# Kernel optimization log

Hardware: AMD Instinct MI355X
Metric: run time of the kernel (lower is better)

The kernel has to match this reference:

```python
import jax, jax.numpy as jnp
import numpy as np

B, N, H, S, NSEC = 1, 8192, 256, 128, 8
TAU = 0.5
DEPTH_LO, DEPTH_HI = 0.0, 2.4
PADDING = 0.1
EPS = 1e-6
_p = float(np.clip(TAU, 1e-4, 1.0 - 1e-4))
LOGIT_TAU = float(np.log(_p / (1.0 - _p)))


def mlp(p, W1, b1, W2, b2, W3, b3, W4, b4):
    # p: [..., 3] -> logit [...]
    h = jax.nn.softplus(p @ W1 + b1)
    h = jax.nn.softplus(h @ W2 + b2)
    h = jax.nn.softplus(h @ W3 + b3)
    return (h @ W4 + b4)[..., 0]


def cube_intersection(ray0, rd):
    # Faithful port of check_ray_intersection_with_unit_cube.
    p_dist = 0.5 + PADDING / 2.0
    plane = jnp.concatenate([jnp.full((3,), p_dist), jnp.full((3,), -p_dist)])  # (6,)
    nom = plane - jnp.tile(ray0, (1, 1, 2))          # (B,N,6)
    den = jnp.tile(rd, (1, 1, 2))
    den = jnp.where(jnp.abs(den) < 1e-9, 1e-9, den)  # numerical guard
    d_int = nom / den                                 # (B,N,6)
    p_int = ray0[:, :, None, :] + d_int[..., None] * rd[:, :, None, :]  # (B,N,6,3)
    inside = jnp.all(jnp.abs(p_int) <= p_dist + EPS, axis=-1)           # (B,N,6)
    mask = inside.sum(-1) == 2                                           # rays hitting cube
    # pick the (exactly two) intersecting planes in ascending plane order,
    # matching torch boolean indexing semantics
    plane_id = jnp.arange(6)
    key = jnp.where(inside, plane_id, plane_id + 6)
    idx2 = jnp.argsort(key, axis=-1)[..., :2]                            # (B,N,2)
    p2 = jnp.take_along_axis(p_int, idx2[..., None], axis=2)            # (B,N,2,3)
    norm_rd = jnp.linalg.norm(rd, axis=-1)                               # (B,N)
    d2 = jnp.linalg.norm(p2 - ray0[:, :, None, :], axis=-1) / norm_rd[..., None]
    d2 = jnp.where(mask[..., None], d2, 0.0)
    d2 = jnp.sort(d2, axis=-1)
    return d2, mask


def _secant(d_low, f_low, d_high, f_high):
    den = f_high - f_low
    den = jnp.where(jnp.abs(den) < 1e-12, 1e-12, den)
    return -f_low * (d_high - d_low) / den + d_low


def reference(ray0, ray_direction, W1, b1, W2, b2, W3, b3, W4, b4):
    rd = ray_direction
    dec = lambda p: mlp(p, W1, b1, W2, b2, W3, b3, W4, b4)
    sg = jax.lax.stop_gradient

    # ---- proposal depths (no grad, as torch no_grad ray-marching) ----
    t = jnp.linspace(0.0, 1.0, S)                       # (S,)
    d_default = DEPTH_LO + t * (DEPTH_HI - DEPTH_LO)
    d2, mask_cube = cube_intersection(ray0, rd)
    d_cube = d2[..., 0:1] + t * (d2[..., 1:2] - d2[..., 0:1])   # (B,N,S)
    d_prop = jnp.where(mask_cube[..., None], d_cube, d_default)
    d_prop = sg(d_prop)

    p_prop = sg(ray0)[:, :, None, :] + d_prop[..., None] * sg(rd)[:, :, None, :]
    val = sg(dec(p_prop)) - LOGIT_TAU                   # (B,N,S)

    mask_0_not_occupied = val[..., 0] < 0
    sign_matrix = jnp.concatenate(
        [jnp.sign(val[..., :-1] * val[..., 1:]), jnp.ones(val.shape[:-1] + (1,), val.dtype)], -1)
    cost = sign_matrix * jnp.arange(S, 0, -1, dtype=val.dtype)
    idx = jnp.argmin(cost, -1)                          # first sign-change step
    vmin = jnp.min(cost, -1)
    f_low = jnp.take_along_axis(val, idx[..., None], -1)[..., 0]
    mask = (vmin < 0) & (f_low < 0) & mask_0_not_occupied

    idx_hi = jnp.minimum(idx + 1, S - 1)
    d_low = jnp.take_along_axis(d_prop, idx[..., None], -1)[..., 0]
    d_high = jnp.take_along_axis(d_prop, idx_hi[..., None], -1)[..., 0]
    f_high = jnp.take_along_axis(val, idx_hi[..., None], -1)[..., 0]

    # ---- secant refinement (no grad in torch) ----
    r0s, rds = sg(ray0), sg(rd)
    d_pred = _secant(d_low, f_low, d_high, f_high)
    for _ in range(NSEC):
        f_mid = sg(dec(r0s + d_pred[..., None] * rds)) - LOGIT_TAU
        low = f_mid < 0
        d_low = jnp.where(low, d_pred, d_low)
        f_low = jnp.where(low, f_mid, f_low)
        d_high = jnp.where(low, d_high, d_pred)
        f_high = jnp.where(low, f_high, f_mid)
        d_pred = _secant(d_low, f_low, d_high, f_high)

    # ---- differentiable implicit-gradient correction (analytic backward of
    # DepthFunction: dd/dtheta = -(df/dtheta)/(df/dd) at the surface point) ----
    d_star = sg(d_pred)
    f_of_d = lambda d: dec(ray0 + d[..., None] * rd) - LOGIT_TAU
    f_val = f_of_d(d_star)                              # differentiable wrt params/rays
    _, df_dd = jax.jvp(f_of_d, (d_star,), (jnp.ones_like(d_star),))
    df_dd = sg(df_dd)
    df_dd = jnp.where(jnp.abs(df_dd) < 1e-6,
                      jnp.where(df_dd < 0, -1e-6, 1e-6), df_dd)
    d_out = d_star - f_val / df_dd
    d_final = jnp.where(mask, d_out, 0.0)
    return d_final


def setup_inputs() -> dict:
    key = jax.random.key(0)
    ks = jax.random.split(key, 10)
    origin = jnp.array([0.0, 0.0, -1.5])
    ray0 = origin + 0.01 * jax.random.normal(ks[0], (B, N, 3), dtype=jnp.float32)
    target = jax.random.uniform(ks[1], (B, N, 3), minval=-0.4, maxval=0.4, dtype=jnp.float32)
    rd = target - ray0
    rd = rd / jnp.linalg.norm(rd, axis=-1, keepdims=True)
    W1 = jax.random.normal(ks[2], (3, H), dtype=jnp.float32) / jnp.sqrt(3.0)
    b1 = 0.1 * jax.random.normal(ks[3], (H,), dtype=jnp.float32)
    W2 = jax.random.normal(ks[4], (H, H), dtype=jnp.float32) / jnp.sqrt(float(H))
    b2 = 0.1 * jax.random.normal(ks[5], (H,), dtype=jnp.float32)
    W3 = jax.random.normal(ks[6], (H, H), dtype=jnp.float32) / jnp.sqrt(float(H))
    b3 = 0.1 * jax.random.normal(ks[7], (H,), dtype=jnp.float32)
    W4 = jax.random.normal(ks[8], (H, 1), dtype=jnp.float32) / jnp.sqrt(float(H))
    b4 = 0.1 * jax.random.normal(ks[9], (1,), dtype=jnp.float32)
    return {"ray0": ray0, "ray_direction": rd, "W1": W1, "b1": b1,
            "W2": W2, "b2": b2, "W3": W3, "b3": b3, "W4": W4, "b4": b4}
```

## Files before the change

### kernel.cpp

```cpp
#include <hip/hip_runtime.h>
#include <math.h>

#define NRAY 8192
#define SSAMP 128
#define HD 256
#define AROW 264
#define A1ROW 40
#define FIXCAP 262144
#define FIXTHR 0.018f

typedef short s16x8 __attribute__((ext_vector_type(8)));
typedef float f32x4 __attribute__((ext_vector_type(4)));

__device__ __forceinline__ unsigned short f2bf(float f) {
    unsigned u = __float_as_uint(f);
    u += 0x7fffu + ((u >> 16) & 1u);
    return (unsigned short)(u >> 16);
}
__device__ __forceinline__ float bf2f(unsigned short s) {
    return __uint_as_float(((unsigned)s) << 16);
}
__device__ __forceinline__ void split2(float f, unsigned short& hi, unsigned short& lo) {
    unsigned u = __float_as_uint(f);
    hi = (unsigned short)(u >> 16);
    float r = f - __uint_as_float(u & 0xFFFF0000u);
    lo = f2bf(r);
}
__device__ __forceinline__ float softplus_fast(float x) {
    return fmaxf(x, 0.0f) + __logf(1.0f + __expf(-fabsf(x)));
}
__device__ __forceinline__ float softplus_cheap(float x) {
    float m = __expf(-fabsf(x));
    float p = fmaf(m, fmaf(0.14258f, m, -0.44943f), 1.0f);
    return fmaxf(x, 0.0f) + m * p;
}
__device__ __forceinline__ float sigmoid_fast(float x) {
    return 1.0f / (1.0f + __expf(-x));
}

__global__ __launch_bounds__(256)
void prep_kernel(const float* __restrict__ W1, const float* __restrict__ b1,
                 const float* __restrict__ W2, const float* __restrict__ W3,
                 const float* __restrict__ ray0, const float* __restrict__ rdg,
                 unsigned short* __restrict__ P2, unsigned short* __restrict__ P3,
                 unsigned short* __restrict__ B1, float* __restrict__ rayinfo,
                 int* __restrict__ fix_cnt) {
    const int b = blockIdx.x, tid = threadIdx.x;
    if (b < 256) {
        int idx = b * 256 + tid;
        int k = idx >> 8, n = idx & 255;
        int nt = n >> 4, kt = k >> 5, lq = (k >> 3) & 3, j = k & 7;
        int lane = (lq << 4) | (n & 15);
        size_t off = (size_t)((nt * 8 + kt) * 2) * 512 + (size_t)lane * 8 + j;
        float w = W2[idx];
        unsigned short hi = f2bf(w);
        P2[off] = hi; P2[off + 512] = f2bf(w - bf2f(hi));
        w = W3[idx];
        hi = f2bf(w);
        P3[off] = hi; P3[off + 512] = f2bf(w - bf2f(hi));
    } else if (b < 288) {
        int idx = (b - 256) * 256 + tid;
        int w = idx & 511;
        int lane = w >> 3, j = w & 7;
        int k = ((lane >> 4) << 3) + j;
        int n = ((idx >> 9) << 4) + (lane & 15);
        unsigned short s = 0;
        if (k < 3) s = f2bf(W1[k * HD + n]);
        else if (k == 3) s = f2bf(b1[n]);
        else if (k < 7) s = f2bf(W1[(k - 4) * HD + n]);
        else if (k == 7) { unsigned short bh = f2bf(b1[n]); s = f2bf(b1[n] - bf2f(bh)); }
        else if (k < 11) { float wv = W1[(k - 8) * HD + n]; unsigned short wh = f2bf(wv); s = f2bf(wv - bf2f(wh)); }
        B1[idx] = s;
    } else {
        int r = (b - 288) * 256 + tid;
        if (r == 0) *fix_cnt = 0;
        float o0 = ray0[3 * r], o1 = ray0[3 * r + 1], o2 = ray0[3 * r + 2];
        float v0 = rdg[3 * r], v1 = rdg[3 * r + 1], v2 = rdg[3 * r + 2];
        const float pd = 0.55f, lim = pd + 1e-6f;
        float di[6]; int insk[6]; int cnt = 0;
        for (int k = 0; k < 6; k++) {
            int a = k % 3;
            float pl = (k < 3) ? pd : -pd;
            float den = (a == 0) ? v0 : ((a == 1) ? v1 : v2);
            if (fabsf(den) < 1e-9f) den = 1e-9f;
            float oa = (a == 0) ? o0 : ((a == 1) ? o1 : o2);
            float dd = (pl - oa) / den;
            float px = o0 + dd * v0, py = o1 + dd * v1, pz = o2 + dd * v2;
            int ins = (fabsf(px) <= lim) && (fabsf(py) <= lim) && (fabsf(pz) <= lim);
            di[k] = dd; insk[k] = ins; cnt += ins;
        }
        float d0 = 0.f, sl = 2.4f;
        if (cnt == 2) {
            int k1 = -1, k2 = -1;
            for (int k = 0; k < 6; k++) if (insk[k]) { if (k1 < 0) k1 = k; else k2 = k; }
            float nrd = sqrtf(v0 * v0 + v1 * v1 + v2 * v2);
            float ax = di[k1] * v0, ay = di[k1] * v1, az = di[k1] * v2;
            float d1n = sqrtf(ax * ax + ay * ay + az * az) / nrd;
            float bx = di[k2] * v0, by = di[k2] * v1, bz = di[k2] * v2;
            float d2n = sqrtf(bx * bx + by * by + bz * bz) / nrd;
            d0 = fminf(d1n, d2n);
            sl = fmaxf(d1n, d2n) - d0;
        }
        float* ri = rayinfo + (size_t)r * 8;
        ri[0] = d0; ri[1] = sl;
        ri[2] = o0; ri[3] = o1; ri[4] = o2;
        ri[5] = v0; ri[6] = v1; ri[7] = v2;
    }
}

template<int MT>
__device__ __forceinline__ void gemm_l1(const unsigned short* A1,
                                        const unsigned short* __restrict__ B1,
                                        f32x4 acc[MT][4], int lane, int ntbase) {
    const int r15 = lane & 15, q = lane >> 4;
    s16x8 bh[4];
#pragma unroll
    for (int nt = 0; nt < 4; nt++)
        bh[nt] = *(((const s16x8*)B1) + (size_t)(ntbase + nt) * 64 + lane);
#pragma unroll
    for (int mt = 0; mt < MT; mt++) {
        s16x8 ah = *(const s16x8*)(A1 + (mt * 16 + r15) * A1ROW + q * 8);
#pragma unroll
        for (int nt = 0; nt < 4; nt++)
            acc[mt][nt] = __builtin_amdgcn_mfma_f32_16x16x32_bf16(ah, bh[nt], (f32x4){0.f,0.f,0.f,0.f}, 0, 0, 0);
    }
}

template<int MT>
__device__ __forceinline__ void gemm_1t(const unsigned short* Ahi,
                                        const unsigned short* __restrict__ Bp,
                                        f32x4 acc[MT][4], int lane, int ntbase) {
#pragma unroll
    for (int mt = 0; mt < MT; mt++)
#pragma unroll
        for (int nt = 0; nt < 4; nt++) acc[mt][nt] = (f32x4){0.f, 0.f, 0.f, 0.f};
    const int r15 = lane & 15, q = lane >> 4;
#pragma unroll 2
    for (int kt = 0; kt < 8; kt++) {
        s16x8 bh[4];
#pragma unroll
        for (int nt = 0; nt < 4; nt++) {
            const s16x8* bp = ((const s16x8*)Bp) + (size_t)((ntbase + nt) * 8 + kt) * 128 + lane;
            bh[nt] = bp[0];
        }
        const int kc = kt * 32 + q * 8;
#pragma unroll
        for (int mt = 0; mt < MT; mt++) {
            s16x8 ah = *(const s16x8*)(Ahi + (mt * 16 + r15) * AROW + kc);
#pragma unroll
            for (int nt = 0; nt < 4; nt++)
                acc[mt][nt] = __builtin_amdgcn_mfma_f32_16x16x32_bf16(ah, bh[nt], acc[mt][nt], 0, 0, 0);
        }
    }
}

template<int MT>
__device__ __forceinline__ void gemm_3t(const unsigned short* Ahi, const unsigned short* Alo,
                                        const unsigned short* __restrict__ Bp,
                                        f32x4 acc[MT][4], int lane, int ntbase) {
#pragma unroll
    for (int mt = 0; mt < MT; mt++)
#pragma unroll
        for (int nt = 0; nt < 4; nt++) acc[mt][nt] = (f32x4){0.f, 0.f, 0.f, 0.f};
    const int r15 = lane & 15, q = lane >> 4;
#pragma unroll 2
    for (int kt = 0; kt < 8; kt++) {
        s16x8 bh[4], bl[4];
#pragma unroll
        for (int nt = 0; nt < 4; nt++) {
            const s16x8* bp = ((const s16x8*)Bp) + (size_t)((ntbase + nt) * 8 + kt) * 128 + lane;
            bh[nt] = bp[0];
            bl[nt] = bp[64];
        }
        const int kc = kt * 32 + q * 8;
#pragma unroll
        for (int mt = 0; mt < MT; mt++) {
            s16x8 ah = *(const s16x8*)(Ahi + (mt * 16 + r15) * AROW + kc);
            s16x8 al = *(const s16x8*)(Alo + (mt * 16 + r15) * AROW + kc);
#pragma unroll
            for (int nt = 0; nt < 4; nt++) {
                acc[mt][nt] = __builtin_amdgcn_mfma_f32_16x16x32_bf16(ah, bh[nt], acc[mt][nt], 0, 0, 0);
                acc[mt][nt] = __builtin_amdgcn_mfma_f32_16x16x32_bf16(ah, bl[nt], acc[mt][nt], 0, 0, 0);
                acc[mt][nt] = __builtin_amdgcn_mfma_f32_16x16x32_bf16(al, bh[nt], acc[mt][nt], 0, 0, 0);
            }
        }
    }
}

template<int MT>
__device__ __forceinline__ void gemm_dual(const unsigned short* Avh, const unsigned short* Avl,
                                          const unsigned short* Ath, const unsigned short* Atl,
                                          const unsigned short* __restrict__ Bp,
                                          f32x4 av[MT][4], f32x4 at[MT][4], int lane, int ntbase) {
#pragma unroll
    for (int mt = 0; mt < MT; mt++)
#pragma unroll
        for (int nt = 0; nt < 4; nt++) {
            av[mt][nt] = (f32x4){0.f, 0.f, 0.f, 0.f};
            at[mt][nt] = (f32x4){0.f, 0.f, 0.f, 0.f};
        }
    const int r15 = lane & 15, q = lane >> 4;
#pragma unroll 2
    for (int kt = 0; kt < 8; kt++) {
        s16x8 bh[4], bl[4];
#pragma unroll
        for (int nt = 0; nt < 4; nt++) {
            const s16x8* bp = ((const s16x8*)Bp) + (size_t)((ntbase + nt) * 8 + kt) * 128 + lane;
            bh[nt] = bp[0];
            bl[nt] = bp[64];
        }
        const int kc = kt * 32 + q * 8;
#pragma unroll
        for (int mt = 0; mt < MT; mt++) {
            s16x8 avh = *(const s16x8*)(Avh + (mt * 16 + r15) * AROW + kc);
            s16x8 avl = *(const s16x8*)(Avl + (mt * 16 + r15) * AROW + kc);
            s16x8 ath = *(const s16x8*)(Ath + (mt * 16 + r15) * AROW + kc);
            s16x8 atl = *(const s16x8*)(Atl + (mt * 16 + r15) * AROW + kc);
#pragma unroll
            for (int nt = 0; nt < 4; nt++) {
                av[mt][nt] = __builtin_amdgcn_mfma_f32_16x16x32_bf16(avh, bh[nt], av[mt][nt], 0, 0, 0);
                av[mt][nt] = __builtin_amdgcn_mfma_f32_16x16x32_bf16(avh, bl[nt], av[mt][nt], 0, 0, 0);
                av[mt][nt] = __builtin_amdgcn_mfma_f32_16x16x32_bf16(avl, bh[nt], av[mt][nt], 0, 0, 0);
                at[mt][nt] = __builtin_amdgcn_mfma_f32_16x16x32_bf16(ath, bh[nt], at[mt][nt], 0, 0, 0);
                at[mt][nt] = __builtin_amdgcn_mfma_f32_16x16x32_bf16(ath, bl[nt], at[mt][nt], 0, 0, 0);
                at[mt][nt] = __builtin_amdgcn_mfma_f32_16x16x32_bf16(atl, bh[nt], at[mt][nt], 0, 0, 0);
            }
        }
    }
}

template<int MT>
__device__ __forceinline__ void epi_l1(f32x4 acc[MT][4], unsigned short* Ahi, int lane, int wn0) {
    const int r15 = lane & 15, q = lane >> 4;
#pragma unroll
    for (int mt = 0; mt < MT; mt++)
#pragma unroll
        for (int nt = 0; nt < 4; nt++) {
            int col = wn0 + nt * 16 + r15;
#pragma unroll
            for (int reg = 0; reg < 4; reg++) {
                int row = mt * 16 + q * 4 + reg;
                Ahi[row * AROW + col] = f2bf(softplus_cheap(acc[mt][nt][reg]));
            }
        }
}

template<int MT>
__device__ __forceinline__ void epi_l1_sp(f32x4 acc[MT][4], unsigned short* Ahi, unsigned short* Alo,
                                          int lane, int wn0) {
    const int r15 = lane & 15, q = lane >> 4;
#pragma unroll
    for (int mt = 0; mt < MT; mt++)
#pragma unroll
        for (int nt = 0; nt < 4; nt++) {
            int col = wn0 + nt * 16 + r15;
#pragma unroll
            for (int reg = 0; reg < 4; reg++) {
                int row = mt * 16 + q * 4 + reg;
                float h = softplus_fast(acc[mt][nt][reg]);
                unsigned short hi, lo;
                split2(h, hi, lo);
                Ahi[row * AROW + col] = hi;
                Alo[row * AROW + col] = lo;
            }
        }
}

template<int MT>
__device__ __forceinline__ void epi_hidden_1t(f32x4 acc[MT][4], const float* __restrict__ b,
                                              unsigned short* Ahi, int lane, int wn0) {
    const int r15 = lane & 15, q = lane >> 4;
#pragma unroll
    for (int mt = 0; mt < MT; mt++)
#pragma unroll
        for (int nt = 0; nt < 4; nt++) {
            int col = wn0 + nt * 16 + r15;
            float bb = b[col];
#pragma unroll
            for (int reg = 0; reg < 4; reg++) {
                int row = mt * 16 + q * 4 + reg;
                Ahi[row * AROW + col] = f2bf(softplus_cheap(acc[mt][nt][reg] + bb));
            }
        }
}

template<int MT>
__device__ __forceinline__ void epi_hidden_sp(f32x4 acc[MT][4], const float* __restrict__ b,
                                              unsigned short* Ahi, unsigned short* Alo,
                                              int lane, int wn0) {
    const int r15 = lane & 15, q = lane >> 4;
#pragma unroll
    for (int mt = 0; mt < MT; mt++)
#pragma unroll
        for (int nt = 0; nt < 4; nt++) {
            int col = wn0 + nt * 16 + r15;
            float bb = b[col];
#pragma unroll
            for (int reg = 0; reg < 4; reg++) {
                int row = mt * 16 + q * 4 + reg;
                float h = softplus_fast(acc[mt][nt][reg] + bb);
                unsigned short hi, lo;
                split2(h, hi, lo);
                Ahi[row * AROW + col] = hi;
                Alo[row * AROW + col] = lo;
            }
        }
}

template<int MT>
__device__ __forceinline__ void epi_dual(f32x4 av[MT][4], f32x4 at[MT][4], const float* __restrict__ b,
                                         unsigned short* Avh, unsigned short* Avl,
                                         unsigned short* Ath, unsigned short* Atl,
                                         int lane, int wn0) {
    const int r15 = lane & 15, q = lane >> 4;
#pragma unroll
    for (int mt = 0; mt < MT; mt++)
#pragma unroll
        for (int nt = 0; nt < 4; nt++) {
            int col = wn0 + nt * 16 + r15;
            float bb = b[col];
#pragma unroll
            for (int reg = 0; reg < 4; reg++) {
                int row = mt * 16 + q * 4 + reg;
                float z = av[mt][nt][reg] + bb;
                float h = softplus_fast(z);
                float ht = sigmoid_fast(z) * at[mt][nt][reg];
                unsigned short hi, lo;
                split2(h, hi, lo);
                Avh[row * AROW + col] = hi;
                Avl[row * AROW + col] = lo;
                split2(ht, hi, lo);
                Ath[row * AROW + col] = hi;
                Atl[row * AROW + col] = lo;
            }
        }
}

template<int MT, bool CH>
__device__ __forceinline__ void l4_reduce(f32x4 acc[MT][4], const float* __restrict__ b3,
                                          const float* __restrict__ W4,
                                          float* partial, int lane, int wn0) {
    const int r15 = lane & 15, q = lane >> 4;
    float w4v[4], b3v[4];
#pragma unroll
    for (int nt = 0; nt < 4; nt++) {
        int col = wn0 + nt * 16 + r15;
        w4v[nt] = W4[col]; b3v[nt] = b3[col];
    }
#pragma unroll
    for (int mt = 0; mt < MT; mt++)
#pragma unroll
        for (int reg = 0; reg < 4; reg++) {
            float p = 0.f;
#pragma unroll
            for (int nt = 0; nt < 4; nt++) {
                float z = acc[mt][nt][reg] + b3v[nt];
                float h = CH ? softplus_cheap(z) : softplus_fast(z);
                p += h * w4v[nt];
            }
#pragma unroll
            for (int m = 1; m < 16; m <<= 1) p += __shfl_xor(p, m, 64);
            if (r15 == 0) partial[mt * 16 + q * 4 + reg] = p;
        }
}

template<int MT>
__device__ __forceinline__ void l4_reduce_dual(f32x4 av[MT][4], f32x4 at[MT][4],
                                               const float* __restrict__ b3, const float* __restrict__ W4,
                                               float* pv, float* pt, int lane, int wn0) {
    const int r15 = lane & 15, q = lane >> 4;
    float w4v[4], b3v[4];
#pragma unroll
    for (int nt = 0; nt < 4; nt++) {
        int col = wn0 + nt * 16 + r15;
        w4v[nt] = W4[col]; b3v[nt] = b3[col];
    }
#pragma unroll
    for (int mt = 0; mt < MT; mt++)
#pragma unroll
        for (int reg = 0; reg < 4; reg++) {
            float sv = 0.f, st = 0.f;
#pragma unroll
            for (int nt = 0; nt < 4; nt++) {
                float z = av[mt][nt][reg] + b3v[nt];
                sv += softplus_fast(z) * w4v[nt];
                st += sigmoid_fast(z) * at[mt][nt][reg] * w4v[nt];
            }
#pragma unroll
            for (int m = 1; m < 16; m <<= 1) {
                sv += __shfl_xor(sv, m, 64);
                st += __shfl_xor(st, m, 64);
            }
            if (r15 == 0) {
                pv[mt * 16 + q * 4 + reg] = sv;
                pt[mt * 16 + q * 4 + reg] = st;
            }
        }
}

__global__ __launch_bounds__(256, 4)
void coarse_mfma(const float* __restrict__ rayinfo,
                 const unsigned short* __restrict__ B1,
                 const unsigned short* __restrict__ P2, const float* __restrict__ b2,
                 const unsigned short* __restrict__ P3, const float* __restrict__ b3,
                 const float* __restrict__ W4, const float* __restrict__ b4,
                 float* __restrict__ val_out, float* __restrict__ dprop_out,
                 int* __restrict__ fix_cnt, int* __restrict__ fix_list) {
    __shared__ __align__(16) unsigned short Ahi[64 * AROW];
    __shared__ __align__(16) unsigned short A1[64 * A1ROW];
    float* partial = (float*)A1;
    const int tid = threadIdx.x;
    const int lane = tid & 63, wave = tid >> 6;
    const int r = blockIdx.x >> 1, half = blockIdx.x & 1;

    if (tid < 64) {
        const float* ri = rayinfo + (size_t)r * 8;
        const int s = half * 64 + tid;
        float t = (float)s * (1.0f / 127.0f);
        float d = fmaf(t, ri[1], ri[0]);
        dprop_out[r * SSAMP + s] = d;
        float px = fmaf(d, ri[5], ri[2]);
        float py = fmaf(d, ri[6], ri[3]);
        float pz = fmaf(d, ri[7], ri[4]);
        unsigned short hx, lx, hy, ly, hz, lz;
        split2(px, hx, lx); split2(py, hy, ly); split2(pz, hz, lz);
        unsigned short* row = A1 + tid * A1ROW;
        row[0] = hx; row[1] = hy; row[2] = hz; row[3] = 0x3F80u;
        row[4] = lx; row[5] = ly; row[6] = lz; row[7] = 0x3F80u;
        row[8] = hx; row[9] = hy; row[10] = hz;
#pragma unroll
        for (int c = 11; c < 32; c++) row[c] = 0;
    }
    __syncthreads();
    f32x4 acc[4][4];
    gemm_l1<4>(A1, B1, acc, lane, wave * 4);
    epi_l1<4>(acc, Ahi, lane, wave * 64);
    __syncthreads();
    gemm_1t<4>(Ahi, P2, acc, lane, wave * 4);
    __syncthreads();
    epi_hidden_1t<4>(acc, b2, Ahi, lane, wave * 64);
    __syncthreads();
    gemm_1t<4>(Ahi, P3, acc, lane, wave * 4);
    l4_reduce<4, true>(acc, b3, W4, &partial[wave * 64], lane, wave * 64);
    __syncthreads();
    if (tid < 64) {
        float v = partial[tid] + partial[64 + tid] + partial[128 + tid] + partial[192 + tid] + b4[0];
        int idx = r * SSAMP + half * 64 + tid;
        val_out[idx] = v;
        if (fabsf(v) < FIXTHR) {
            int pos = atomicAdd(fix_cnt, 1);
            if (pos < FIXCAP) fix_list[pos] = idx;
        }
    }
}

__global__ __launch_bounds__(256, 4)
void fixup3_mfma(const int* __restrict__ counter, const int* __restrict__ list,
                 float* __restrict__ val, const float* __restrict__ dprop,
                 const float* __restrict__ ray0, const float* __restrict__ rdg,
                 const unsigned short* __restrict__ B1,
                 const unsigned short* __restrict__ P2, const float* __restrict__ b2,
                 const unsigned short* __restrict__ P3, const float* __restrict__ b3,
                 const float* __restrict__ W4, const float* __restrict__ b4) {
    __shared__ __align__(16) unsigned short Ahi[32 * AROW];
    __shared__ __align__(16) unsigned short Alo[32 * AROW];
    __shared__ __align__(16) unsigned short A1[32 * A1ROW];
    __shared__ float partial[4][32];
    __shared__ int bidxs[32];
    const int cnt = min(*counter, FIXCAP);
    const int base = blockIdx.x * 32;
    if (base >= cnt) return;
    const int tid = threadIdx.x;
    const int lane = tid & 63, wave = tid >> 6;
    if (tid < 32) {
        const int i = min(base + tid, cnt - 1);
        const int bidx = list[i];
        bidxs[tid] = bidx;
        const int rr = bidx >> 7;
        float d = dprop[bidx];
        float px = ray0[3 * rr] + d * rdg[3 * rr];
        float py = ray0[3 * rr + 1] + d * rdg[3 * rr + 1];
        float pz = ray0[3 * rr + 2] + d * rdg[3 * rr + 2];
        unsigned short hx, lx, hy, ly, hz, lz;
        split2(px, hx, lx); split2(py, hy, ly); split2(pz, hz, lz);
        unsigned short* row = A1 + tid * A1ROW;
        row[0] = hx; row[1] = hy; row[2] = hz; row[3] = 0x3F80u;
        row[4] = lx; row[5] = ly; row[6] = lz; row[7] = 0x3F80u;
        row[8] = hx; row[9] = hy; row[10] = hz;
#pragma unroll
        for (int c = 11; c < 32; c++) row[c] = 0;
    }
    __syncthreads();
    f32x4 acc[2][4];
    gemm_l1<2>(A1, B1, acc, lane, wave * 4);
    epi_l1_sp<2>(acc, Ahi, Alo, lane, wave * 64);
    __syncthreads();
    gemm_3t<2>(Ahi, Alo, P2, acc, lane, wave * 4);
    __syncthreads();
    epi_hidden_sp<2>(acc, b2, Ahi, Alo, lane, wave * 64);
    __syncthreads();
    gemm_3t<2>(Ahi, Alo, P3, acc, lane, wave * 4);
    l4_reduce<2, false>(acc, b3, W4, &partial[wave][0], lane, wave * 64);
    __syncthreads();
    if (tid < 32) {
        float v = partial[0][tid] + partial[1][tid] + partial[2][tid] + partial[3][tid] + b4[0];
        val[bidxs[tid]] = v;
    }
}

__global__ __launch_bounds__(256, 4)
void refine_mfma(const float* __restrict__ val, const float* __restrict__ dprop,
                 const float* __restrict__ ray0, const float* __restrict__ rdg,
                 const float* __restrict__ W1, const float* __restrict__ b1,
                 const unsigned short* __restrict__ P2, const float* __restrict__ b2,
                 const unsigned short* __restrict__ P3, const float* __restrict__ b3,
                 const float* __restrict__ W4, const float* __restrict__ b4,
                 float* __restrict__ out) {
    __shared__ __align__(16) unsigned short Avh[16 * AROW];
    __shared__ __align__(16) unsigned short Avl[16 * AROW];
    __shared__ __align__(16) unsigned short Ath[16 * AROW];
    __shared__ __align__(16) unsigned short Atl[16 * AROW];
    __shared__ float partial[4][16], ptan[4][16];
    __shared__ float dl[16], fl[16], dh[16], fh[16], dps[16];
    __shared__ int mks[16];
    unsigned short* Ahi = Avh;
    const int tid = threadIdx.x;
    const int lane = tid & 63, wave = tid >> 6;
    const int r0 = blockIdx.x * 16;

    for (int i = 0; i < 4; i++) {
        const int r = r0 + wave * 4 + i;
        const float2 v = *(const float2*)(val + (size_t)r * SSAMP + lane * 2);
        const float2 dd = *(const float2*)(dprop + (size_t)r * SSAMP + lane * 2);
        float vnext = __shfl_down(v.x, 1, 64);
        const int s0 = lane * 2, s1 = s0 + 1;
        float pr0 = v.x * v.y;
        int sg0 = (pr0 > 0.f) ? 1 : ((pr0 < 0.f) ? -1 : 0);
        int k0 = (sg0 * (SSAMP - s0) + 129) * 256 + s0;
        int k1;
        if (lane == 63) {
            k1 = (1 + 129) * 256 + 127;
        } else {
            float pr1 = v.y * vnext;
            int sg1 = (pr1 > 0.f) ? 1 : ((pr1 < 0.f) ? -1 : 0);
            k1 = (sg1 * (SSAMP - s1) + 129) * 256 + s1;
        }
        int k = min(k0, k1);
#pragma unroll
        for (int m = 1; m < 64; m <<= 1) k = min(k, __shfl_xor(k, m, 64));
        int bidx = k & 255;
        int cmin = (k >> 8) - 129;
        int idxh = min(bidx + 1, SSAMP - 1);
        int ow = bidx >> 1, oh = idxh >> 1;
        float fa = __shfl(v.x, ow, 64), fb = __shfl(v.y, ow, 64);
        float da = __shfl(dd.x, ow, 64), db = __shfl(dd.y, ow, 64);
        float fa2 = __shfl(v.x, oh, 64), fb2 = __shfl(v.y, oh, 64);
        float da2 = __shfl(dd.x, oh, 64), db2 = __shfl(dd.y, oh, 64);
        float v0 = __shfl(v.x, 0, 64);
        if (lane == 0) {
            float f_low = (bidx & 1) ? fb : fa;
            float d_low = (bidx & 1) ? db : da;
            float f_high = (idxh & 1) ? fb2 : fa2;
            float d_high = (idxh & 1) ? db2 : da2;
            int sl = wave * 4 + i;
            mks[sl] = (cmin < 0) && (f_low < 0.f) && (v0 < 0.f);
            float den = f_high - f_low;
            if (fabsf(den) < 1e-12f) den = 1e-12f;
            dl[sl] = d_low; fl[sl] = f_low; dh[sl] = d_high; fh[sl] = f_high;
            dps[sl] = -f_low * (d_high - d_low) / den + d_low;
        }
    }
    __syncthreads();
    for (int it = 0; it < 8; it++) {
        {
            const int pt = tid >> 4, jb = (tid & 15) << 4;
            const int rr = r0 + pt;
            float d = dps[pt];
            float px = ray0[3 * rr] + d * rdg[3 * rr];
            float py = ray0[3 * rr + 1] + d * rdg[3 * rr + 1];
            float pz = ray0[3 * rr + 2] + d * rdg[3 * rr + 2];
            for (int j = jb; j < jb + 16; j += 4) {
                float4 wa = *(const float4*)(W1 + j);
                float4 wb = *(const float4*)(W1 + 256 + j);
                float4 wc = *(const float4*)(W1 + 512 + j);
                float4 bb = *(const float4*)(b1 + j);
                float z[4];
                z[0] = fmaf(px, wa.x, fmaf(py, wb.x, fmaf(pz, wc.x, bb.x)));
                z[1] = fmaf(px, wa.y, fmaf(py, wb.y, fmaf(pz, wc.y, bb.y)));
                z[2] = fmaf(px, wa.z, fmaf(py, wb.z, fmaf(pz, wc.z, bb.z)));
                z[3] = fmaf(px, wa.w, fmaf(py, wb.w, fmaf(pz, wc.w, bb.w)));
#pragma unroll
                for (int i = 0; i < 4; i++)
                    Ahi[pt * AROW + j + i] = f2bf(softplus_cheap(z[i]));
            }
        }
        __syncthreads();
        f32x4 acc[1][4];
        gemm_1t<1>(Ahi, P2, acc, lane, wave * 4);
        __syncthreads();
        epi_hidden_1t<1>(acc, b2, Ahi, lane, wave * 64);
        __syncthreads();
        gemm_1t<1>(Ahi, P3, acc, lane, wave * 4);
        l4_reduce<1, true>(acc, b3, W4, &partial[wave][0], lane, wave * 64);
        __syncthreads();
        if (tid < 16) {
            float fm = partial[0][tid] + partial[1][tid] + partial[2][tid] + partial[3][tid] + b4[0];
            float dpv = dps[tid];
            float dlv = dl[tid], flv = fl[tid], dhv = dh[tid], fhv = fh[tid];
            if (fm < 0.f) { dlv = dpv; flv = fm; } else { dhv = dpv; fhv = fm; }
            float den = fhv - flv;
            if (fabsf(den) < 1e-12f) den = 1e-12f;
            dps[tid] = -flv * (dhv - dlv) / den + dlv;
            dl[tid] = dlv; fl[tid] = flv; dh[tid] = dhv; fh[tid] = fhv;
        }
        __syncthreads();
    }
    {
        const int pt = tid >> 4, jb = (tid & 15) << 4;
        const int rr = r0 + pt;
        float d = dps[pt];
        float v0 = rdg[3 * rr], v1 = rdg[3 * rr + 1], v2 = rdg[3 * rr + 2];
        float px = ray0[3 * rr] + d * v0;
        float py = ray0[3 * rr + 1] + d * v1;
        float pz = ray0[3 * rr + 2] + d * v2;
        for (int j = jb; j < jb + 16; j += 4) {
            float4 wa = *(const float4*)(W1 + j);
            float4 wb = *(const float4*)(W1 + 256 + j);
            float4 wc = *(const float4*)(W1 + 512 + j);
            float4 bb = *(const float4*)(b1 + j);
            float z[4], zt[4];
            z[0] = fmaf(px, wa.x, fmaf(py, wb.x, fmaf(pz, wc.x, bb.x)));
            z[1] = fmaf(px, wa.y, fmaf(py, wb.y, fmaf(pz, wc.y, bb.y)));
            z[2] = fmaf(px, wa.z, fmaf(py, wb.z, fmaf(pz, wc.z, bb.z)));
            z[3] = fmaf(px, wa.w, fmaf(py, wb.w, fmaf(pz, wc.w, bb.w)));
            zt[0] = fmaf(v0, wa.x, fmaf(v1, wb.x, v2 * wc.x));
            zt[1] = fmaf(v0, wa.y, fmaf(v1, wb.y, v2 * wc.y));
            zt[2] = fmaf(v0, wa.z, fmaf(v1, wb.z, v2 * wc.z));
            zt[3] = fmaf(v0, wa.w, fmaf(v1, wb.w, v2 * wc.w));
#pragma unroll
            for (int i = 0; i < 4; i++) {
                float h = softplus_fast(z[i]);
                float ht = sigmoid_fast(z[i]) * zt[i];
                unsigned short hi, lo;
                split2(h, hi, lo);
                Avh[pt * AROW + j + i] = hi;
                Avl[pt * AROW + j + i] = lo;
                split2(ht, hi, lo);
                Ath[pt * AROW + j + i] = hi;
                Atl[pt * AROW + j + i] = lo;
            }
        }
    }
    __syncthreads();
    f32x4 av[1][4], at[1][4];
    gemm_dual<1>(Avh, Avl, Ath, Atl, P2, av, at, lane, wave * 4);
    __syncthreads();
    epi_dual<1>(av, at, b2, Avh, Avl, Ath, Atl, lane, wave * 64);
    __syncthreads();
    gemm_dual<1>(Avh, Avl, Ath, Atl, P3, av, at, lane, wave * 4);
    l4_reduce_dual<1>(av, at, b3, W4, &partial[wave][0], &ptan[wave][0], lane, wave * 64);
    __syncthreads();
    if (tid < 16) {
        float f = partial[0][tid] + partial[1][tid] + partial[2][tid] + partial[3][tid] + b4[0];
        float ft = ptan[0][tid] + ptan[1][tid] + ptan[2][tid] + ptan[3][tid];
        if (fabsf(ft) < 1e-6f) ft = (ft < 0.f) ? -1e-6f : 1e-6f;
        float dres = dps[tid] - f / ft;
        out[r0 + tid] = mks[tid] ? dres : 0.0f;
    }
}

extern "C" void kernel_launch(void* const* d_in, const int* in_sizes, int n_in,
                              void* d_out, int out_size, void* d_ws, size_t ws_size,
                              hipStream_t stream) {
    const float* ray0 = (const float*)d_in[0];
    const float* rdg  = (const float*)d_in[1];
    const float* W1 = (const float*)d_in[2];
    const float* b1 = (const float*)d_in[3];
    const float* W2 = (const float*)d_in[4];
    const float* b2 = (const float*)d_in[5];
    const float* W3 = (const float*)d_in[6];
    const float* b3 = (const float*)d_in[7];
    const float* W4 = (const float*)d_in[8];
    const float* b4 = (const float*)d_in[9];
    float* out = (float*)d_out;

    float* ws = (float*)d_ws;
    float* val    = ws;
    float* dprop  = ws + (size_t)SSAMP * NRAY;
    unsigned short* P2 = (unsigned short*)(ws + (size_t)2 * SSAMP * NRAY);
    unsigned short* P3 = P2 + 131072;
    unsigned short* B1 = P3 + 131072;
    float* rayinfo = (float*)(B1 + 8192);
    int* fix_cnt  = (int*)(rayinfo + (size_t)NRAY * 8);
    int* fix_list = fix_cnt + 64;

    hipLaunchKernelGGL(prep_kernel, dim3(320), dim3(256), 0, stream,
                       W1, b1, W2, W3, ray0, rdg, P2, P3, B1, rayinfo, fix_cnt);
    hipLaunchKernelGGL(coarse_mfma, dim3(NRAY * 2), dim3(256), 0, stream,
                       rayinfo, B1, P2, b2, P3, b3, W4, b4, val, dprop, fix_cnt, fix_list);
    hipLaunchKernelGGL(fixup3_mfma, dim3(FIXCAP / 32), dim3(256), 0, stream,
                       fix_cnt, fix_list, val, dprop, ray0, rdg,
                       B1, P2, b2, P3, b3, W4, b4);
    hipLaunchKernelGGL(refine_mfma, dim3(NRAY / 16), dim3(256), 0, stream,
                       val, dprop, ray0, rdg, W1, b1, P2, b2, P3, b3, W4, b4, out);
}
```

Measured before the change: 726.3 us.

## Transpose MFMA operand order and vectorize epilogue stores with packed bf16 conversion

Swaps the A/B operands of every MFMA so each lane's accumulator holds four consecutive hidden columns of one row instead of four rows of one column. Epilogues can then write packed 64-bit stores to LDS using the hardware v_cvt_pk_bf16_f32 instruction in place of scalar 16-bit stores, and bias/W4 loads become vector loads. The final-layer reduction needs only two cross-lane shuffles instead of four. The change also alters bf16 rounding for the hi part (round-to-nearest instead of truncation), so the hi/lo split numerics differ slightly.

```diff
diff --git a/kernel.cpp b/kernel.cpp
--- a/kernel.cpp
+++ b/kernel.cpp
@@ -25,6 +25,11 @@
     hi = (unsigned short)(u >> 16);
     float r = f - __uint_as_float(u & 0xFFFF0000u);
     lo = f2bf(r);
+}
+__device__ __forceinline__ unsigned pack_bf16x2(float a, float b) {
+    unsigned r;
+    asm("v_cvt_pk_bf16_f32 %0, %1, %2" : "=v"(r) : "v"(a), "v"(b));
+    return r;
 }
 __device__ __forceinline__ float softplus_fast(float x) {
     return fmaxf(x, 0.0f) + __logf(1.0f + __expf(-fabsf(x)));
@@ -108,27 +113,28 @@
     }
 }
 
+
 template<int MT>
 __device__ __forceinline__ void gemm_l1(const unsigned short* A1,
                                         const unsigned short* __restrict__ B1,
                                         f32x4 acc[MT][4], int lane, int ntbase) {
     const int r15 = lane & 15, q = lane >> 4;
-    s16x8 bh[4];
+    s16x8 wh[4];
 #pragma unroll
     for (int nt = 0; nt < 4; nt++)
-        bh[nt] = *(((const s16x8*)B1) + (size_t)(ntbase + nt) * 64 + lane);
+        wh[nt] = *(((const s16x8*)B1) + (size_t)(ntbase + nt) * 64 + lane);
 #pragma unroll
     for (int mt = 0; mt < MT; mt++) {
         s16x8 ah = *(const s16x8*)(A1 + (mt * 16 + r15) * A1ROW + q * 8);
 #pragma unroll
         for (int nt = 0; nt < 4; nt++)
-            acc[mt][nt] = __builtin_amdgcn_mfma_f32_16x16x32_bf16(ah, bh[nt], (f32x4){0.f,0.f,0.f,0.f}, 0, 0, 0);
-    }
-}
-
-template<int MT>
-__device__ __forceinline__ void gemm_1t(const unsigned short* Ahi,
-                                        const unsigned short* __restrict__ Bp,
+            acc[mt][nt] = __builtin_amdgcn_mfma_f32_16x16x32_bf16(wh[nt], ah, (f32x4){0.f,0.f,0.f,0.f}, 0, 0, 0);
+    }
+}
+
+template<int MT>
+__device__ __forceinline__ void gemm_1t(const unsigned short* Act,
+                                        const unsigned short* __restrict__ Wp,
                                         f32x4 acc[MT][4], int lane, int ntbase) {
 #pragma unroll
     for (int mt = 0; mt < MT; mt++)
@@ -137,26 +143,26 @@
     const int r15 = lane & 15, q = lane >> 4;
 #pragma unroll 2
     for (int kt = 0; kt < 8; kt++) {
-        s16x8 bh[4];
-#pragma unroll
-        for (int nt = 0; nt < 4; nt++) {
-            const s16x8* bp = ((const s16x8*)Bp) + (size_t)((ntbase + nt) * 8 + kt) * 128 + lane;
-            bh[nt] = bp[0];
+        s16x8 wh[4];
+#pragma unroll
+        for (int nt = 0; nt < 4; nt++) {
+            const s16x8* wp = ((const s16x8*)Wp) + (size_t)((ntbase + nt) * 8 + kt) * 128 + lane;
+            wh[nt] = wp[0];
         }
         const int kc = kt * 32 + q * 8;
 #pragma unroll
         for (int mt = 0; mt < MT; mt++) {
-            s16x8 ah = *(const s16x8*)(Ahi + (mt * 16 + r15) * AROW + kc);
+            s16x8 ah = *(const s16x8*)(Act + (mt * 16 + r15) * AROW + kc);
 #pragma unroll
             for (int nt = 0; nt < 4; nt++)
-                acc[mt][nt] = __builtin_amdgcn_mfma_f32_16x16x32_bf16(ah, bh[nt], acc[mt][nt], 0, 0, 0);
+                acc[mt][nt] = __builtin_amdgcn_mfma_f32_16x16x32_bf16(wh[nt], ah, acc[mt][nt], 0, 0, 0);
         }
     }
 }
 
 template<int MT>
 __device__ __forceinline__ void gemm_3t(const unsigned short* Ahi, const unsigned short* Alo,
-                                        const unsigned short* __restrict__ Bp,
+                                        const unsigned short* __restrict__ Wp,
                                         f32x4 acc[MT][4], int lane, int ntbase) {
 #pragma unroll
     for (int mt = 0; mt < MT; mt++)
@@ -165,12 +171,12 @@
     const int r15 = lane & 15, q = lane >> 4;
 #pragma unroll 2
     for (int kt = 0; kt < 8; kt++) {
-        s16x8 bh[4], bl[4];
-#pragma unroll
-        for (int nt = 0; nt < 4; nt++) {
-            const s16x8* bp = ((const s16x8*)Bp) + (size_t)((ntbase + nt) * 8 + kt) * 128 + lane;
-            bh[nt] = bp[0];
-            bl[nt] = bp[64];
+        s16x8 wh[4], wl[4];
+#pragma unroll
+        for (int nt = 0; nt < 4; nt++) {
+            const s16x8* wp = ((const s16x8*)Wp) + (size_t)((ntbase + nt) * 8 + kt) * 128 + lane;
+            wh[nt] = wp[0];
+            wl[nt] = wp[64];
         }
         const int kc = kt * 32 + q * 8;
 #pragma unroll
@@ -179,9 +185,9 @@
             s16x8 al = *(const s16x8*)(Alo + (mt * 16 + r15) * AROW + kc);
 #pragma unroll
             for (int nt = 0; nt < 4; nt++) {
-                acc[mt][nt] = __builtin_amdgcn_mfma_f32_16x16x32_bf16(ah, bh[nt], acc[mt][nt], 0, 0, 0);
-                acc[mt][nt] = __builtin_amdgcn_mfma_f32_16x16x32_bf16(ah, bl[nt], acc[mt][nt], 0, 0, 0);
-                acc[mt][nt] = __builtin_amdgcn_mfma_f32_16x16x32_bf16(al, bh[nt], acc[mt][nt], 0, 0, 0);
+                acc[mt][nt] = __builtin_amdgcn_mfma_f32_16x16x32_bf16(wh[nt], ah, acc[mt][nt], 0, 0, 0);
+                acc[mt][nt] = __builtin_amdgcn_mfma_f32_16x16x32_bf16(wl[nt], ah, acc[mt][nt], 0, 0, 0);
+                acc[mt][nt] = __builtin_amdgcn_mfma_f32_16x16x32_bf16(wh[nt], al, acc[mt][nt], 0, 0, 0);
             }
         }
     }
@@ -190,7 +196,7 @@
 template<int MT>
 __device__ __forceinline__ void gemm_dual(const unsigned short* Avh, const unsigned short* Avl,
                                           const unsigned short* Ath, const unsigned short* Atl,
-                                          const unsigned short* __restrict__ Bp,
+                                          const unsigned short* __restrict__ Wp,
                                           f32x4 av[MT][4], f32x4 at[MT][4], int lane, int ntbase) {
 #pragma unroll
     for (int mt = 0; mt < MT; mt++)
@@ -202,28 +208,28 @@
     const int r15 = lane & 15, q = lane >> 4;
 #pragma unroll 2
     for (int kt = 0; kt < 8; kt++) {
-        s16x8 bh[4], bl[4];
-#pragma unroll
-        for (int nt = 0; nt < 4; nt++) {
-            const s16x8* bp = ((const s16x8*)Bp) + (size_t)((ntbase + nt) * 8 + kt) * 128 + lane;
-            bh[nt] = bp[0];
-            bl[nt] = bp[64];
+        s16x8 wh[4], wl[4];
+#pragma unroll
+        for (int nt = 0; nt < 4; nt++) {
+            const s16x8* wp = ((const s16x8*)Wp) + (size_t)((ntbase + nt) * 8 + kt) * 128 + lane;
+            wh[nt] = wp[0];
+            wl[nt] = wp[64];
         }
         const int kc = kt * 32 + q * 8;
 #pragma unroll
         for (int mt = 0; mt < MT; mt++) {
-            s16x8 avh = *(const s16x8*)(Avh + (mt * 16 + r15) * AROW + kc);
-            s16x8 avl = *(const s16x8*)(Avl + (mt * 16 + r15) * AROW + kc);
-            s16x8 ath = *(const s16x8*)(Ath + (mt * 16 + r15) * AROW + kc);
-            s16x8 atl = *(const s16x8*)(Atl + (mt * 16 + r15) * AROW + kc);
+            s16x8 avhf = *(const s16x8*)(Avh + (mt * 16 + r15) * AROW + kc);
+            s16x8 avlf = *(const s16x8*)(Avl + (mt * 16 + r15) * AROW + kc);
+            s16x8 athf = *(const s16x8*)(Ath + (mt * 16 + r15) * AROW + kc);
+            s16x8 atlf = *(const s16x8*)(Atl + (mt * 16 + r15) * AROW + kc);
 #pragma unroll
             for (int nt = 0; nt < 4; nt++) {
-                av[mt][nt] = __builtin_amdgcn_mfma_f32_16x16x32_bf16(avh, bh[nt], av[mt][nt], 0, 0, 0);
-                av[mt][nt] = __builtin_amdgcn_mfma_f32_16x16x32_bf16(avh, bl[nt], av[mt][nt], 0, 0, 0);
-                av[mt][nt] = __builtin_amdgcn_mfma_f32_16x16x32_bf16(avl, bh[nt], av[mt][nt], 0, 0, 0);
-                at[mt][nt] = __builtin_amdgcn_mfma_f32_16x16x32_bf16(ath, bh[nt], at[mt][nt], 0, 0, 0);
-                at[mt][nt] = __builtin_amdgcn_mfma_f32_16x16x32_bf16(ath, bl[nt], at[mt][nt], 0, 0, 0);
-                at[mt][nt] = __builtin_amdgcn_mfma_f32_16x16x32_bf16(atl, bh[nt], at[mt][nt], 0, 0, 0);
+                av[mt][nt] = __builtin_amdgcn_mfma_f32_16x16x32_bf16(wh[nt], avhf, av[mt][nt], 0, 0, 0);
+                av[mt][nt] = __builtin_amdgcn_mfma_f32_16x16x32_bf16(wl[nt], avhf, av[mt][nt], 0, 0, 0);
+                av[mt][nt] = __builtin_amdgcn_mfma_f32_16x16x32_bf16(wh[nt], avlf, av[mt][nt], 0, 0, 0);
+                at[mt][nt] = __builtin_amdgcn_mfma_f32_16x16x32_bf16(wh[nt], athf, at[mt][nt], 0, 0, 0);
+                at[mt][nt] = __builtin_amdgcn_mfma_f32_16x16x32_bf16(wl[nt], athf, at[mt][nt], 0, 0, 0);
+                at[mt][nt] = __builtin_amdgcn_mfma_f32_16x16x32_bf16(wh[nt], atlf, at[mt][nt], 0, 0, 0);
             }
         }
     }
@@ -233,16 +239,18 @@
 __device__ __forceinline__ void epi_l1(f32x4 acc[MT][4], unsigned short* Ahi, int lane, int wn0) {
     const int r15 = lane & 15, q = lane >> 4;
 #pragma unroll
-    for (int mt = 0; mt < MT; mt++)
-#pragma unroll
-        for (int nt = 0; nt < 4; nt++) {
-            int col = wn0 + nt * 16 + r15;
-#pragma unroll
-            for (int reg = 0; reg < 4; reg++) {
-                int row = mt * 16 + q * 4 + reg;
-                Ahi[row * AROW + col] = f2bf(softplus_cheap(acc[mt][nt][reg]));
-            }
-        }
+    for (int mt = 0; mt < MT; mt++) {
+        unsigned short* rowp = Ahi + (mt * 16 + r15) * AROW + wn0 + q * 4;
+#pragma unroll
+        for (int nt = 0; nt < 4; nt++) {
+            float h0 = softplus_cheap(acc[mt][nt][0]);
+            float h1 = softplus_cheap(acc[mt][nt][1]);
+            float h2 = softplus_cheap(acc[mt][nt][2]);
+            float h3 = softplus_cheap(acc[mt][nt][3]);
+            *reinterpret_cast<uint2*>(rowp + nt * 16) =
+                make_uint2(pack_bf16x2(h0, h1), pack_bf16x2(h2, h3));
+        }
+    }
 }
 
 template<int MT>
@@ -250,38 +258,46 @@
                                           int lane, int wn0) {
     const int r15 = lane & 15, q = lane >> 4;
 #pragma unroll
-    for (int mt = 0; mt < MT; mt++)
-#pragma unroll
-        for (int nt = 0; nt < 4; nt++) {
-            int col = wn0 + nt * 16 + r15;
-#pragma unroll
-            for (int reg = 0; reg < 4; reg++) {
-                int row = mt * 16 + q * 4 + reg;
-                float h = softplus_fast(acc[mt][nt][reg]);
-                unsigned short hi, lo;
-                split2(h, hi, lo);
-                Ahi[row * AROW + col] = hi;
-                Alo[row * AROW + col] = lo;
-            }
-        }
+    for (int mt = 0; mt < MT; mt++) {
+        const int rowoff = (mt * 16 + r15) * AROW + wn0 + q * 4;
+#pragma unroll
+        for (int nt = 0; nt < 4; nt++) {
+            float h0 = softplus_fast(acc[mt][nt][0]);
+            float h1 = softplus_fast(acc[mt][nt][1]);
+            float h2 = softplus_fast(acc[mt][nt][2]);
+            float h3 = softplus_fast(acc[mt][nt][3]);
+            unsigned x0 = pack_bf16x2(h0, h1), x1 = pack_bf16x2(h2, h3);
+            float l0 = h0 - __uint_as_float(x0 << 16);
+            float l1 = h1 - __uint_as_float(x0 & 0xFFFF0000u);
+            float l2 = h2 - __uint_as_float(x1 << 16);
+            float l3 = h3 - __uint_as_float(x1 & 0xFFFF0000u);
+            *reinterpret_cast<uint2*>(Ahi + rowoff + nt * 16) = make_uint2(x0, x1);
+            *reinterpret_cast<uint2*>(Alo + rowoff + nt * 16) =
+                make_uint2(pack_bf16x2(l0, l1), pack_bf16x2(l2, l3));
+        }
+    }
 }
 
 template<int MT>
 __device__ __forceinline__ void epi_hidden_1t(f32x4 acc[MT][4], const float* __restrict__ b,
                                               unsigned short* Ahi, int lane, int wn0) {
     const int r15 = lane & 15, q = lane >> 4;
-#pragma unroll
-    for (int mt = 0; mt < MT; mt++)
-#pragma unroll
-        for (int nt = 0; nt < 4; nt++) {
-            int col = wn0 + nt * 16 + r15;
-            float bb = b[col];
-#pragma unroll
-            for (int reg = 0; reg < 4; reg++) {
-                int row = mt * 16 + q * 4 + reg;
-                Ahi[row * AROW + col] = f2bf(softplus_cheap(acc[mt][nt][reg] + bb));
-            }
-        }
+    f32x4 bb[4];
+#pragma unroll
+    for (int nt = 0; nt < 4; nt++) bb[nt] = *(const f32x4*)(b + wn0 + nt * 16 + q * 4);
+#pragma unroll
+    for (int mt = 0; mt < MT; mt++) {
+        unsigned short* rowp = Ahi + (mt * 16 + r15) * AROW + wn0 + q * 4;
+#pragma unroll
+        for (int nt = 0; nt < 4; nt++) {
+            float h0 = softplus_cheap(acc[mt][nt][0] + bb[nt][0]);
+            float h1 = softplus_cheap(acc[mt][nt][1] + bb[nt][1]);
+            float h2 = softplus_cheap(acc[mt][nt][2] + bb[nt][2]);
+            float h3 = softplus_cheap(acc[mt][nt][3] + bb[nt][3]);
+            *reinterpret_cast<uint2*>(rowp + nt * 16) =
+                make_uint2(pack_bf16x2(h0, h1), pack_bf16x2(h2, h3));
+        }
+    }
 }
 
 template<int MT>
@@ -289,22 +305,28 @@
                                               unsigned short* Ahi, unsigned short* Alo,
                                               int lane, int wn0) {
     const int r15 = lane & 15, q = lane >> 4;
-#pragma unroll
-    for (int mt = 0; mt < MT; mt++)
-#pragma unroll
-        for (int nt = 0; nt < 4; nt++) {
-            int col = wn0 + nt * 16 + r15;
-            float bb = b[col];
-#pragma unroll
-            for (int reg = 0; reg < 4; reg++) {
-                int row = mt * 16 + q * 4 + reg;
-                float h = softplus_fast(acc[mt][nt][reg] + bb);
-                unsigned short hi, lo;
-                split2(h, hi, lo);
-                Ahi[row * AROW + col] = hi;
-                Alo[row * AROW + col] = lo;
-            }
-        }
+    f32x4 bb[4];
+#pragma unroll
+    for (int nt = 0; nt < 4; nt++) bb[nt] = *(const f32x4*)(b + wn0 + nt * 16 + q * 4);
+#pragma unroll
+    for (int mt = 0; mt < MT; mt++) {
+        const int rowoff = (mt * 16 + r15) * AROW + wn0 + q * 4;
+#pragma unroll
+        for (int nt = 0; nt < 4; nt++) {
+            float h0 = softplus_fast(acc[mt][nt][0] + bb[nt][0]);
+            float h1 = softplus_fast(acc[mt][nt][1] + bb[nt][1]);
+            float h2 = softplus_fast(acc[mt][nt][2] + bb[nt][2]);
+            float h3 = softplus_fast(acc[mt][nt][3] + bb[nt][3]);
+            unsigned x0 = pack_bf16x2(h0, h1), x1 = pack_bf16x2(h2, h3);
+            float l0 = h0 - __uint_as_float(x0 << 16);
+            float l1 = h1 - __uint_as_float(x0 & 0xFFFF0000u);
+            float l2 = h2 - __uint_as_float(x1 << 16);
+            float l3 = h3 - __uint_as_float(x1 & 0xFFFF0000u);
+            *reinterpret_cast<uint2*>(Ahi + rowoff + nt * 16) = make_uint2(x0, x1);
+            *reinterpret_cast<uint2*>(Alo + rowoff + nt * 16) =
+                make_uint2(pack_bf16x2(l0, l1), pack_bf16x2(l2, l3));
+        }
+    }
 }
 
 template<int MT>
@@ -313,27 +335,39 @@
                                          unsigned short* Ath, unsigned short* Atl,
                                          int lane, int wn0) {
     const int r15 = lane & 15, q = lane >> 4;
-#pragma unroll
-    for (int mt = 0; mt < MT; mt++)
-#pragma unroll
-        for (int nt = 0; nt < 4; nt++) {
-            int col = wn0 + nt * 16 + r15;
-            float bb = b[col];
-#pragma unroll
-            for (int reg = 0; reg < 4; reg++) {
-                int row = mt * 16 + q * 4 + reg;
-                float z = av[mt][nt][reg] + bb;
-                float h = softplus_fast(z);
-                float ht = sigmoid_fast(z) * at[mt][nt][reg];
-                unsigned short hi, lo;
-                split2(h, hi, lo);
-                Avh[row * AROW + col] = hi;
-                Avl[row * AROW + col] = lo;
-                split2(ht, hi, lo);
-                Ath[row * AROW + col] = hi;
-                Atl[row * AROW + col] = lo;
+    f32x4 bb[4];
+#pragma unroll
+    for (int nt = 0; nt < 4; nt++) bb[nt] = *(const f32x4*)(b + wn0 + nt * 16 + q * 4);
+#pragma unroll
+    for (int mt = 0; mt < MT; mt++) {
+        const int rowoff = (mt * 16 + r15) * AROW + wn0 + q * 4;
+#pragma unroll
+        for (int nt = 0; nt < 4; nt++) {
+            float h[4], g[4];
+#pragma unroll
+            for (int r = 0; r < 4; r++) {
+                float z = av[mt][nt][r] + bb[nt][r];
+                h[r] = softplus_fast(z);
+                g[r] = sigmoid_fast(z) * at[mt][nt][r];
             }
-        }
+            unsigned x0 = pack_bf16x2(h[0], h[1]), x1 = pack_bf16x2(h[2], h[3]);
+            float l0 = h[0] - __uint_as_float(x0 << 16);
+            float l1 = h[1] - __uint_as_float(x0 & 0xFFFF0000u);
+            float l2 = h[2] - __uint_as_float(x1 << 16);
+            float l3 = h[3] - __uint_as_float(x1 & 0xFFFF0000u);
+            *reinterpret_cast<uint2*>(Avh + rowoff + nt * 16) = make_uint2(x0, x1);
+            *reinterpret_cast<uint2*>(Avl + rowoff + nt * 16) =
+                make_uint2(pack_bf16x2(l0, l1), pack_bf16x2(l2, l3));
+            x0 = pack_bf16x2(g[0], g[1]); x1 = pack_bf16x2(g[2], g[3]);
+            l0 = g[0] - __uint_as_float(x0 << 16);
+            l1 = g[1] - __uint_as_float(x0 & 0xFFFF0000u);
+            l2 = g[2] - __uint_as_float(x1 << 16);
+            l3 = g[3] - __uint_as_float(x1 & 0xFFFF0000u);
+            *reinterpret_cast<uint2*>(Ath + rowoff + nt * 16) = make_uint2(x0, x1);
+            *reinterpret_cast<uint2*>(Atl + rowoff + nt * 16) =
+                make_uint2(pack_bf16x2(l0, l1), pack_bf16x2(l2, l3));
+        }
+    }
 }
 
 template<int MT, bool CH>
@@ -341,27 +375,27 @@
                                           const float* __restrict__ W4,
                                           float* partial, int lane, int wn0) {
     const int r15 = lane & 15, q = lane >> 4;
-    float w4v[4], b3v[4];
+    f32x4 w4v[4], b3v[4];
 #pragma unroll
     for (int nt = 0; nt < 4; nt++) {
-        int col = wn0 + nt * 16 + r15;
-        w4v[nt] = W4[col]; b3v[nt] = b3[col];
-    }
-#pragma unroll
-    for (int mt = 0; mt < MT; mt++)
-#pragma unroll
-        for (int reg = 0; reg < 4; reg++) {
-            float p = 0.f;
-#pragma unroll
-            for (int nt = 0; nt < 4; nt++) {
-                float z = acc[mt][nt][reg] + b3v[nt];
+        w4v[nt] = *(const f32x4*)(W4 + wn0 + nt * 16 + q * 4);
+        b3v[nt] = *(const f32x4*)(b3 + wn0 + nt * 16 + q * 4);
+    }
+#pragma unroll
+    for (int mt = 0; mt < MT; mt++) {
+        float p = 0.f;
+#pragma unroll
+        for (int nt = 0; nt < 4; nt++)
+#pragma unroll
+            for (int r = 0; r < 4; r++) {
+                float z = acc[mt][nt][r] + b3v[nt][r];
                 float h = CH ? softplus_cheap(z) : softplus_fast(z);
-                p += h * w4v[nt];
+                p = fmaf(h, w4v[nt][r], p);
             }
-#pragma unroll
-            for (int m = 1; m < 16; m <<= 1) p += __shfl_xor(p, m, 64);
-            if (r15 == 0) partial[mt * 16 + q * 4 + reg] = p;
-        }
+        p += __shfl_xor(p, 16, 64);
+        p += __shfl_xor(p, 32, 64);
+        if (q == 0) partial[mt * 16 + r15] = p;
+    }
 }
 
 template<int MT>
@@ -369,33 +403,32 @@
                                                const float* __restrict__ b3, const float* __restrict__ W4,
                                                float* pv, float* pt, int lane, int wn0) {
     const int r15 = lane & 15, q = lane >> 4;
-    float w4v[4], b3v[4];
+    f32x4 w4v[4], b3v[4];
 #pragma unroll
     for (int nt = 0; nt < 4; nt++) {
-        int col = wn0 + nt * 16 + r15;
-        w4v[nt] = W4[col]; b3v[nt] = b3[col];
-    }
-#pragma unroll
-    for (int mt = 0; mt < MT; mt++)
-#pragma unroll
-        for (int reg = 0; reg < 4; reg++) {
-            float sv = 0.f, st = 0.f;
-#pragma unroll
-            for (int nt = 0; nt < 4; nt++) {
-                float z = av[mt][nt][reg] + b3v[nt];
-                sv += softplus_fast(z) * w4v[nt];
-                st += sigmoid_fast(z) * at[mt][nt][reg] * w4v[nt];
+        w4v[nt] = *(const f32x4*)(W4 + wn0 + nt * 16 + q * 4);
+        b3v[nt] = *(const f32x4*)(b3 + wn0 + nt * 16 + q * 4);
+    }
+#pragma unroll
+    for (int mt = 0; mt < MT; mt++) {
+        float sv = 0.f, st = 0.f;
+#pragma unroll
+        for (int nt = 0; nt < 4; nt++)
+#pragma unroll
+            for (int r = 0; r < 4; r++) {
+                float z = av[mt][nt][r] + b3v[nt][r];
+                sv = fmaf(softplus_fast(z), w4v[nt][r], sv);
+                st = fmaf(sigmoid_fast(z) * at[mt][nt][r], w4v[nt][r], st);
             }
-#pragma unroll
-            for (int m = 1; m < 16; m <<= 1) {
-                sv += __shfl_xor(sv, m, 64);
-                st += __shfl_xor(st, m, 64);
-            }
-            if (r15 == 0) {
-                pv[mt * 16 + q * 4 + reg] = sv;
-                pt[mt * 16 + q * 4 + reg] = st;
-            }
-        }
+        sv += __shfl_xor(sv, 16, 64);
+        sv += __shfl_xor(sv, 32, 64);
+        st += __shfl_xor(st, 16, 64);
+        st += __shfl_xor(st, 32, 64);
+        if (q == 0) {
+            pv[mt * 16 + r15] = sv;
+            pt[mt * 16 + r15] = st;
+        }
+    }
 }
 
 __global__ __launch_bounds__(256, 4)
@@ -589,9 +622,9 @@
                 z[1] = fmaf(px, wa.y, fmaf(py, wb.y, fmaf(pz, wc.y, bb.y)));
                 z[2] = fmaf(px, wa.z, fmaf(py, wb.z, fmaf(pz, wc.z, bb.z)));
                 z[3] = fmaf(px, wa.w, fmaf(py, wb.w, fmaf(pz, wc.w, bb.w)));
-#pragma unroll
-                for (int i = 0; i < 4; i++)
-                    Ahi[pt * AROW + j + i] = f2bf(softplus_cheap(z[i]));
+                *reinterpret_cast<uint2*>(&Ahi[pt * AROW + j]) =
+                    make_uint2(pack_bf16x2(softplus_cheap(z[0]), softplus_cheap(z[1])),
+                               pack_bf16x2(softplus_cheap(z[2]), softplus_cheap(z[3])));
             }
         }
         __syncthreads();
@@ -628,7 +661,7 @@
             float4 wb = *(const float4*)(W1 + 256 + j);
             float4 wc = *(const float4*)(W1 + 512 + j);
             float4 bb = *(const float4*)(b1 + j);
-            float z[4], zt[4];
+            float z[4], zt[4], h[4], g[4];
             z[0] = fmaf(px, wa.x, fmaf(py, wb.x, fmaf(pz, wc.x, bb.x)));
             z[1] = fmaf(px, wa.y, fmaf(py, wb.y, fmaf(pz, wc.y, bb.y)));
             z[2] = fmaf(px, wa.z, fmaf(py, wb.z, fmaf(pz, wc.z, bb.z)));
@@ -639,16 +672,25 @@
             zt[3] = fmaf(v0, wa.w, fmaf(v1, wb.w, v2 * wc.w));
 #pragma unroll
             for (int i = 0; i < 4; i++) {
-                float h = softplus_fast(z[i]);
-                float ht = sigmoid_fast(z[i]) * zt[i];
-                unsigned short hi, lo;
-                split2(h, hi, lo);
-                Avh[pt * AROW + j + i] = hi;
-                Avl[pt * AROW + j + i] = lo;
-                split2(ht, hi, lo);
-                Ath[pt * AROW + j + i] = hi;
-                Atl[pt * AROW + j + i] = lo;
+                h[i] = softplus_fast(z[i]);
+                g[i] = sigmoid_fast(z[i]) * zt[i];
             }
+            unsigned x0 = pack_bf16x2(h[0], h[1]), x1 = pack_bf16x2(h[2], h[3]);
+            float l0 = h[0] - __uint_as_float(x0 << 16);
+            float l1 = h[1] - __uint_as_float(x0 & 0xFFFF0000u);
+            float l2 = h[2] - __uint_as_float(x1 << 16);
+            float l3 = h[3] - __uint_as_float(x1 & 0xFFFF0000u);
+            *reinterpret_cast<uint2*>(&Avh[pt * AROW + j]) = make_uint2(x0, x1);
+            *reinterpret_cast<uint2*>(&Avl[pt * AROW + j]) =
+                make_uint2(pack_bf16x2(l0, l1), pack_bf16x2(l2, l3));
+            x0 = pack_bf16x2(g[0], g[1]); x1 = pack_bf16x2(g[2], g[3]);
+            l0 = g[0] - __uint_as_float(x0 << 16);
+            l1 = g[1] - __uint_as_float(x0 & 0xFFFF0000u);
+            l2 = g[2] - __uint_as_float(x1 << 16);
+            l3 = g[3] - __uint_as_float(x1 & 0xFFFF0000u);
+            *reinterpret_cast<uint2*>(&Ath[pt * AROW + j]) = make_uint2(x0, x1);
+            *reinterpret_cast<uint2*>(&Atl[pt * AROW + j]) =
+                make_uint2(pack_bf16x2(l0, l1), pack_bf16x2(l2, l3));
         }
     }
     __syncthreads();
```

Result: faster. 708.5 us (-2.4%).
